# Kernel tuning notes

Hardware: AMD Instinct MI355X
Metric: run time of the kernel (lower is better)

## Reference

```python
import jax, jax.numpy as jnp
import numpy as np
import math

TOKEN_DIM = 1024
NUM_HEADS = 16
HEAD_DIM = TOKEN_DIM // NUM_HEADS
T, B, N = 32, 32, 64


def setup_inputs() -> dict:
    key = jax.random.key(0)
    ks = jax.random.split(key, 9)
    query_vec = jax.random.normal(ks[0], (T, B, TOKEN_DIM), dtype=jnp.float32)
    tokens = jax.random.normal(ks[1], (T, B, N, TOKEN_DIM), dtype=jnp.float32)
    gate_logits = jax.random.normal(ks[2], (T, B, N), dtype=jnp.float32)
    scale = 1.0 / math.sqrt(TOKEN_DIM)
    Wq = jax.random.normal(ks[3], (TOKEN_DIM, TOKEN_DIM), dtype=jnp.float32) * scale
    Wk = jax.random.normal(ks[4], (TOKEN_DIM, TOKEN_DIM), dtype=jnp.float32) * scale
    Wv = jax.random.normal(ks[5], (TOKEN_DIM, TOKEN_DIM), dtype=jnp.float32) * scale
    bq = jnp.zeros((TOKEN_DIM,), dtype=jnp.float32)
    bk = jnp.zeros((TOKEN_DIM,), dtype=jnp.float32)
    bv = jnp.zeros((TOKEN_DIM,), dtype=jnp.float32)
    return {"query_vec": query_vec, "tokens": tokens, "gate_logits": gate_logits,
            "Wq": Wq, "bq": bq, "Wk": Wk, "bk": bk, "Wv": Wv, "bv": bv}


def reference(query_vec, tokens, gate_logits, Wq, bq, Wk, bk, Wv, bv):
    # QKV projections
    q = query_vec @ Wq + bq                      # [T,B,D]
    k = tokens @ Wk + bk                         # [T,B,N,D]
    v = tokens @ Wv + bv                         # [T,B,N,D]
    q = q.reshape(T, B, NUM_HEADS, HEAD_DIM)
    k = k.reshape(T, B, N, NUM_HEADS, HEAD_DIM)
    v = v.reshape(T, B, N, NUM_HEADS, HEAD_DIM)
    logits = jnp.einsum('tbhd,tbnhd->tbhn', q, k) / math.sqrt(HEAD_DIM)
    logits = logits + gate_logits[:, :, None, :]
    attn = jax.nn.softmax(logits, axis=-1)       # [T,B,H,N]
    attended = jnp.einsum('tbhn,tbnhd->tbhd', attn, v)
    attended = attended.reshape(T, B, TOKEN_DIM)
    mean_attn = attn.mean(axis=2)                # [T,B,N]
    return (attended, mean_attn, logits)
```

## Files before the change

### kernel.cpp

```cpp
#include <hip/hip_runtime.h>
#include <hip/hip_bf16.h>
#include <hip/hip_cooperative_groups.h>

namespace cg = cooperative_groups;

typedef __attribute__((ext_vector_type(4))) float f32x4;
typedef __attribute__((ext_vector_type(8))) short bf16x8;
typedef unsigned int u32;
typedef unsigned short u16;

#define DEV static __device__ __forceinline__


DEV u16 f2bf(float x){
  union { float f; u32 u; } v; v.f = x;
  u32 r = v.u + 0x7FFFu + ((v.u >> 16) & 1u);
  return (u16)(r >> 16);
}
DEV float bf2f(u16 s){
  union { u32 u; float f; } v; v.u = ((u32)s) << 16;
  return v.f;
}

#define MFMA16(a,b,c) __builtin_amdgcn_mfma_f32_16x16x32_bf16((a),(b),(c),0,0,0)

DEV int tok_off(int n, int dbyte){ return n*2048 + (dbyte ^ ((n & 7) << 4)); }

#define MEGA_DYN_LDS 65536

__global__ __launch_bounds__(256, 2) void k_mega(
    const float* __restrict__ qv, const float* __restrict__ tokens,
    const float* __restrict__ gate,
    const float* __restrict__ Wq, const float* __restrict__ bq,
    const float* __restrict__ Wk, const float* __restrict__ bk,
    const float* __restrict__ Wv, const float* __restrict__ bv,
    u16* __restrict__ qvB, u16* __restrict__ WqT, u16* __restrict__ WkB,
    u16* __restrict__ WvT, float* __restrict__ qf, u16* __restrict__ qb,
    u16* __restrict__ U, u16* __restrict__ ctxb,
    float* __restrict__ out_att, float* __restrict__ out_mean,
    float* __restrict__ out_logits){
  extern __shared__ __align__(16) char smem[];
  __shared__ __align__(16) char sstat[10496];
  cg::grid_group grid = cg::this_grid();
  const int tid = threadIdx.x;
  const int bx  = blockIdx.x;
  const int l = tid & 63, w = tid >> 6, g = l >> 4, li = l & 15;

  {
    const f32x4* s4 = (const f32x4*)qv;
    uint2* d2 = (uint2*)qvB;
    int g0 = bx*256 + tid;
    #pragma unroll
    for (int i = 0; i < 2; ++i){
      int idx = g0 + i*131072;
      f32x4 v = s4[idx];
      uint2 pk;
      pk.x = (u32)f2bf(v.x) | ((u32)f2bf(v.y) << 16);
      pk.y = (u32)f2bf(v.z) | ((u32)f2bf(v.w) << 16);
      d2[idx] = pk;
    }
  }
  {
    u16 (*tile)[65] = (u16 (*)[65])sstat;
    for (int tl = bx; tl < 768; tl += 512){
      __syncthreads();
      const int which = tl >> 8, t8 = tl & 255;
      const float* src = which==0 ? Wq : (which==1 ? Wk : Wv);
      const int bi = (t8 >> 4) << 6, bj = (t8 & 15) << 6;
      #pragma unroll
      for (int k2 = 0; k2 < 16; ++k2){
        int e = tid + (k2 << 8); int r = e >> 6, c = e & 63;
        tile[r][c] = f2bf(src[(size_t)(bi + r)*1024 + bj + c]);
      }
      __syncthreads();
      if (which == 1){
        #pragma unroll
        for (int k2 = 0; k2 < 16; ++k2){
          int e = tid + (k2 << 8); int r = e >> 6, c = e & 63;
          WkB[(size_t)(bi + r)*1024 + bj + c] = tile[r][c];
        }
      } else {
        u16* dst = which==0 ? WqT : WvT;
        #pragma unroll
        for (int k2 = 0; k2 < 16; ++k2){
          int e = tid + (k2 << 8); int r = e >> 6, c = e & 63;
          dst[(size_t)(bj + r)*1024 + bi + c] = tile[c][r];
        }
      }
    }
  }
  __threadfence(); grid.sync(); __threadfence();

  {
    const int wm = w & 1, wn = w >> 1;
    const int m_base = (bx >> 5)*64 + wm*32;
    const int n_base = (bx & 31)*32 + wn*16;
    f32x4 acc[2]; acc[0] = (f32x4)0.0f; acc[1] = (f32x4)0.0f;
    #pragma unroll 4
    for (int kb = 0; kb < 32; ++kb){
      const int k0 = kb*32 + g*8;
      bf16x8 b = *(const bf16x8*)(WqT + (size_t)(n_base + li)*1024 + k0);
      #pragma unroll
      for (int rt = 0; rt < 2; ++rt){
        bf16x8 a = *(const bf16x8*)(qvB + (size_t)(m_base + rt*16 + li)*1024 + k0);
        acc[rt] = MFMA16(a, b, acc[rt]);
      }
    }
    #pragma unroll
    for (int rt = 0; rt < 2; ++rt)
      #pragma unroll
      for (int r = 0; r < 4; ++r){
        int m = m_base + rt*16 + g*4 + r;
        int n = n_base + li;
        float val = acc[rt][r] + bq[n];
        qf[(size_t)m*1024 + n] = val;
        qb[(size_t)m*1024 + n] = f2bf(val);
      }
  }
  __threadfence(); grid.sync(); __threadfence();

  {
    u16 (*stile)[64] = (u16 (*)[64])sstat;
    const int wm = w & 1, wn = w >> 1;
    for (int i = 0; i < 8; ++i){
      const int tl = bx*8 + i;
      const int tb0 = (tl >> 8)*64, d0 = ((tl >> 4) & 15)*64, h = tl & 15;
      f32x4 acc[2][2];
      #pragma unroll
      for (int a0=0;a0<2;++a0)
        #pragma unroll
        for (int b0=0;b0<2;++b0) acc[a0][b0] = (f32x4)0.0f;
      #pragma unroll
      for (int kb = 0; kb < 2; ++kb){
        const int k0 = h*64 + kb*32 + g*8;
        bf16x8 a[2], b[2];
        #pragma unroll
        for (int rt=0;rt<2;++rt)
          a[rt] = *(const bf16x8*)(qb + (size_t)(tb0 + wm*32 + rt*16 + li)*1024 + k0);
        #pragma unroll
        for (int ct=0;ct<2;++ct)
          b[ct] = *(const bf16x8*)(WkB + (size_t)(d0 + wn*32 + ct*16 + li)*1024 + k0);
        #pragma unroll
        for (int rt=0;rt<2;++rt)
          #pragma unroll
          for (int ct=0;ct<2;++ct)
            acc[rt][ct] = MFMA16(a[rt], b[ct], acc[rt][ct]);
      }
      __syncthreads();
      #pragma unroll
      for (int rt=0;rt<2;++rt)
        #pragma unroll
        for (int ct=0;ct<2;++ct)
          #pragma unroll
          for (int r=0;r<4;++r)
            stile[wm*32 + rt*16 + g*4 + r][wn*32 + ct*16 + li] = f2bf(acc[rt][ct][r]);
      __syncthreads();
      const int rr = tid >> 2, cg4 = tid & 3;
      f32x4* dst = (f32x4*)(U + ((size_t)(tb0 + rr)*16 + h)*1024 + d0 + cg4*16);
      const f32x4* s4 = (const f32x4*)(&stile[rr][cg4*16]);
      dst[0] = s4[0]; dst[1] = s4[1];
    }
  }
  __threadfence(); grid.sync(); __threadfence();

  {
    float* part_s   = (float*)(sstat);
    float* logits_s = (float*)(sstat + 4096);
    float* p_s      = (float*)(sstat + 8192);
    float* csum     = (float*)(sstat + 10240);
    float* r_s      = (float*)(sstat + 10304);
    float* mzs      = (float*)(sstat + 10368);
    const int nt = w & 1, kh = w >> 1;
    const int sh = tid >> 4, sj = tid & 15;

    __syncthreads();

    {
      const f32x4* src4 = (const f32x4*)(tokens + (size_t)bx*65536);
      f32x4 pstg[32];
      #pragma unroll
      for (int it = 0; it < 32; ++it) pstg[it] = src4[(size_t)it*256 + tid];
      #pragma unroll
      for (int it = 0; it < 32; ++it){
        f32x4 v = pstg[it];
        uint2 pk;
        pk.x = (u32)f2bf(v.x) | ((u32)f2bf(v.y) << 16);
        pk.y = (u32)f2bf(v.z) | ((u32)f2bf(v.w) << 16);
        *(uint2*)(smem + tok_off(it, tid*8)) = pk;
      }
    }

    float m_run = -1e30f, z_run = 0.0f;
    f32x4 cacc[4][4];

    for (int r = 0; r < 4; ++r){
      const int c = r & 1, n0 = c*32;
      const int tb = bx + (r >> 1)*512;

      if (c == 0){
        m_run = -1e30f; z_run = 0.0f;
        #pragma unroll
        for (int i=0;i<4;++i)
          #pragma unroll
          for (int j=0;j<4;++j) cacc[i][j] = (f32x4)0.0f;
        const float* qp = qf + (size_t)tb*1024 + sh*64 + sj*4;
        const float* bp = bk + sh*64 + sj*4;
        float part = qp[0]*bp[0] + qp[1]*bp[1] + qp[2]*bp[2] + qp[3]*bp[3];
        part += __shfl_xor(part, 1); part += __shfl_xor(part, 2);
        part += __shfl_xor(part, 4); part += __shfl_xor(part, 8);
        if (sj == 0) csum[sh] = part;
      }

      __syncthreads();

      {
        bf16x8 a[16];
        const bf16x8* Ub = (const bf16x8*)(U + (size_t)tb*16384);
        #pragma unroll
        for (int i = 0; i < 16; ++i)
          a[i] = Ub[li*128 + (kh*16 + i)*4 + g];
        f32x4 acc = (f32x4)0.0f;
        #pragma unroll
        for (int i = 0; i < 16; ++i){
          int kb = kh*16 + i;
          bf16x8 b = *(const bf16x8*)(smem + tok_off(nt*16 + li, (kb*32 + g*8)*2));
          acc = MFMA16(a[i], b, acc);
        }
        *(f32x4*)(part_s + (size_t)(w*64 + l)*4) = acc;
        __syncthreads();
        if (kh == 0){
          acc += *(const f32x4*)(part_s + (size_t)((w+2)*64 + l)*4);
          float gv = gate[(size_t)tb*64 + n0 + nt*16 + li];
          #pragma unroll
          for (int rg = 0; rg < 4; ++rg){
            int h = g*4 + rg;
            logits_s[h*64 + n0 + nt*16 + li] = (acc[rg] + csum[h])*0.125f + gv;
          }
        }
        __syncthreads();
      }

      f32x4 stg[32];
      const int rn = r + 1;
      if (rn < 4){
        const f32x4* srcn = (const f32x4*)(tokens + (size_t)(bx + (rn >> 1)*512)*65536);
        const int n0n = (rn & 1)*32;
        #pragma unroll
        for (int it = 0; it < 32; ++it)
          stg[it] = srcn[(size_t)(n0n + it)*256 + tid];
      }

      {
        float lv0 = logits_s[sh*64 + n0 + sj];
        float lv1 = logits_s[sh*64 + n0 + 16 + sj];
        out_logits[(size_t)tb*1024 + sh*64 + n0 + sj]      = lv0;
        out_logits[(size_t)tb*1024 + sh*64 + n0 + 16 + sj] = lv1;
        float cm = fmaxf(lv0, lv1);
        cm = fmaxf(cm, __shfl_xor(cm, 1)); cm = fmaxf(cm, __shfl_xor(cm, 2));
        cm = fmaxf(cm, __shfl_xor(cm, 4)); cm = fmaxf(cm, __shfl_xor(cm, 8));
        float m_new = fmaxf(m_run, cm);
        float rsc = __expf(m_run - m_new);
        float p0 = __expf(lv0 - m_new), p1 = __expf(lv1 - m_new);
        float zs = p0 + p1;
        zs += __shfl_xor(zs, 1); zs += __shfl_xor(zs, 2);
        zs += __shfl_xor(zs, 4); zs += __shfl_xor(zs, 8);
        z_run = z_run * rsc + zs;
        m_run = m_new;
        p_s[sj*16 + sh]        = p0;
        p_s[(sj + 16)*16 + sh] = p1;
        if (sj == 0){
          r_s[sh] = rsc;
          if (c == 1){ mzs[sh*2] = m_new; mzs[sh*2 + 1] = 1.0f / z_run; }
        }
      }
      __syncthreads();

      {
        float rr[4];
        #pragma unroll
        for (int hh = 0; hh < 4; ++hh) rr[hh] = r_s[w*4 + hh];
        #pragma unroll
        for (int dq = 0; dq < 4; ++dq)
          #pragma unroll
          for (int hh = 0; hh < 4; ++hh) cacc[dq][hh] *= rr[hh];
        for (int nl = 0; nl < 32; ++nl){
          f32x4 p = *(const f32x4*)(p_s + nl*16 + w*4);
          #pragma unroll
          for (int dq = 0; dq < 4; ++dq){
            uint2 t2 = *(const uint2*)(smem + tok_off(nl, (dq*256 + l*4)*2));
            float f0 = bf2f((u16)(t2.x & 0xFFFFu));
            float f1 = bf2f((u16)(t2.x >> 16));
            float f2 = bf2f((u16)(t2.y & 0xFFFFu));
            float f3 = bf2f((u16)(t2.y >> 16));
            #pragma unroll
            for (int hh = 0; hh < 4; ++hh){
              float av = p[hh];
              cacc[dq][hh].x += av*f0; cacc[dq][hh].y += av*f1;
              cacc[dq][hh].z += av*f2; cacc[dq][hh].w += av*f3;
            }
          }
        }
      }
      __syncthreads();

      if (rn < 4){
        #pragma unroll
        for (int it = 0; it < 32; ++it){
          f32x4 v = stg[it];
          uint2 pk;
          pk.x = (u32)f2bf(v.x) | ((u32)f2bf(v.y) << 16);
          pk.y = (u32)f2bf(v.z) | ((u32)f2bf(v.w) << 16);
          *(uint2*)(smem + tok_off(it, tid*8)) = pk;
        }
      }

      if (c == 1){
        if (tid < 64){
          float s = 0.0f;
          #pragma unroll
          for (int h = 0; h < 16; ++h)
            s += __expf(logits_s[h*64 + tid] - mzs[h*2]) * mzs[h*2 + 1];
          out_mean[(size_t)tb*64 + tid] = s * 0.0625f;
        }
        #pragma unroll
        for (int hh = 0; hh < 4; ++hh){
          const int h = w*4 + hh;
          const float zinv = mzs[h*2 + 1];
          #pragma unroll
          for (int dq = 0; dq < 4; ++dq){
            f32x4 v = cacc[dq][hh];
            uint2 pk;
            pk.x = (u32)f2bf(v.x * zinv) | ((u32)f2bf(v.y * zinv) << 16);
            pk.y = (u32)f2bf(v.z * zinv) | ((u32)f2bf(v.w * zinv) << 16);
            *(uint2*)(ctxb + ((size_t)tb*16 + h)*1024 + dq*256 + l*4) = pk;
          }
        }
      }
    }
  }
  __threadfence(); grid.sync(); __threadfence();

  {
    const int wm = w & 1, wn = w >> 1;
    const int m_base = (bx >> 4)*32, h = bx & 15;
    f32x4 acc[2]; acc[0] = (f32x4)0.0f; acc[1] = (f32x4)0.0f;
    #pragma unroll 4
    for (int kb = 0; kb < 32; ++kb){
      const int k0 = kb*32 + g*8;
      bf16x8 a = *(const bf16x8*)(ctxb + ((size_t)(m_base + wm*16 + li)*16 + h)*1024 + k0);
      #pragma unroll
      for (int ct = 0; ct < 2; ++ct){
        bf16x8 b = *(const bf16x8*)(WvT + (size_t)(h*64 + wn*32 + ct*16 + li)*1024 + k0);
        acc[ct] = MFMA16(a, b, acc[ct]);
      }
    }
    #pragma unroll
    for (int ct = 0; ct < 2; ++ct)
      #pragma unroll
      for (int r = 0; r < 4; ++r){
        int m = m_base + wm*16 + g*4 + r;
        int dout = h*64 + wn*32 + ct*16 + li;
        out_att[(size_t)m*1024 + dout] = acc[ct][r] + bv[dout];
      }
  }
}

__global__ __launch_bounds__(256) void k_convert(
    const float* __restrict__ Wq, const float* __restrict__ Wk, const float* __restrict__ Wv,
    u16* __restrict__ WqT, u16* __restrict__ WkB, u16* __restrict__ WvT){
  __shared__ u16 tile[64][65];
  const int which = blockIdx.y;
  const float* src = which==0 ? Wq : (which==1 ? Wk : Wv);
  const int bi = (blockIdx.x >> 4) << 6;
  const int bj = (blockIdx.x & 15) << 6;
  const int t  = threadIdx.x;
  #pragma unroll
  for (int k2 = 0; k2 < 16; ++k2){
    int e = t + (k2 << 8);
    int r = e >> 6, c = e & 63;
    tile[r][c] = f2bf(src[(size_t)(bi + r)*1024 + bj + c]);
  }
  __syncthreads();
  if (which == 1){
    #pragma unroll
    for (int k2 = 0; k2 < 16; ++k2){
      int e = t + (k2 << 8); int r = e >> 6, c = e & 63;
      WkB[(size_t)(bi + r)*1024 + bj + c] = tile[r][c];
    }
  } else {
    u16* dst = which==0 ? WqT : WvT;
    #pragma unroll
    for (int k2 = 0; k2 < 16; ++k2){
      int e = t + (k2 << 8); int r = e >> 6, c = e & 63;
      dst[(size_t)(bj + r)*1024 + bi + c] = tile[c][r];
    }
  }
}

__global__ __launch_bounds__(256) void k_qproj(
    const float* __restrict__ qv, const u16* __restrict__ WqT, const float* __restrict__ bq,
    float* __restrict__ qf, u16* __restrict__ qb){
  const int l = threadIdx.x & 63, w = threadIdx.x >> 6;
  const int wm = w & 1, wn = w >> 1;
  const int g = l >> 4, li = l & 15;
  const int m_base = blockIdx.x*64 + wm*32;
  const int n_base = blockIdx.y*64 + wn*32;
  f32x4 acc[2][2];
  #pragma unroll
  for (int i=0;i<2;++i)
    #pragma unroll
    for (int j=0;j<2;++j) acc[i][j] = (f32x4)0.0f;

  #pragma unroll 4
  for (int kb = 0; kb < 32; ++kb){
    const int k0 = kb*32 + g*8;
    bf16x8 a[2], b[2];
    #pragma unroll
    for (int rt = 0; rt < 2; ++rt){
      const float* p = qv + (size_t)(m_base + rt*16 + li)*1024 + k0;
      f32x4 lo = *(const f32x4*)p;
      f32x4 hi = *(const f32x4*)(p+4);
      union { u16 s[8]; bf16x8 v; } u;
      u.s[0]=f2bf(lo.x); u.s[1]=f2bf(lo.y); u.s[2]=f2bf(lo.z); u.s[3]=f2bf(lo.w);
      u.s[4]=f2bf(hi.x); u.s[5]=f2bf(hi.y); u.s[6]=f2bf(hi.z); u.s[7]=f2bf(hi.w);
      a[rt] = u.v;
    }
    #pragma unroll
    for (int ct = 0; ct < 2; ++ct)
      b[ct] = *(const bf16x8*)(WqT + (size_t)(n_base + ct*16 + li)*1024 + k0);
    #pragma unroll
    for (int rt = 0; rt < 2; ++rt)
      #pragma unroll
      for (int ct = 0; ct < 2; ++ct)
        acc[rt][ct] = MFMA16(a[rt], b[ct], acc[rt][ct]);
  }
  #pragma unroll
  for (int rt=0;rt<2;++rt)
    #pragma unroll
    for (int ct=0;ct<2;++ct)
      #pragma unroll
      for (int r=0;r<4;++r){
        int m = m_base + rt*16 + g*4 + r;
        int n = n_base + ct*16 + li;
        float val = acc[rt][ct][r] + bq[n];
        qf[(size_t)m*1024 + n] = val;
        qb[(size_t)m*1024 + n] = f2bf(val);
      }
}

__global__ __launch_bounds__(256) void k_umat(
    const u16* __restrict__ qb, const u16* __restrict__ WkB, u16* __restrict__ U){
  __shared__ __align__(16) u16 stile[64][64];
  const int l = threadIdx.x & 63, w = threadIdx.x >> 6;
  const int wm = w & 1, wn = w >> 1, g = l >> 4, li = l & 15;
  const int tb0 = blockIdx.x*64, d0 = blockIdx.y*64, h = blockIdx.z;
  f32x4 acc[2][2];
  #pragma unroll
  for (int i=0;i<2;++i)
    #pragma unroll
    for (int j=0;j<2;++j) acc[i][j] = (f32x4)0.0f;

  #pragma unroll
  for (int kb = 0; kb < 2; ++kb){
    const int k0 = h*64 + kb*32 + g*8;
    bf16x8 a[2], b[2];
    #pragma unroll
    for (int rt=0;rt<2;++rt)
      a[rt] = *(const bf16x8*)(qb + (size_t)(tb0 + wm*32 + rt*16 + li)*1024 + k0);
    #pragma unroll
    for (int ct=0;ct<2;++ct)
      b[ct] = *(const bf16x8*)(WkB + (size_t)(d0 + wn*32 + ct*16 + li)*1024 + k0);
    #pragma unroll
    for (int rt=0;rt<2;++rt)
      #pragma unroll
      for (int ct=0;ct<2;++ct)
        acc[rt][ct] = MFMA16(a[rt], b[ct], acc[rt][ct]);
  }
  #pragma unroll
  for (int rt=0;rt<2;++rt)
    #pragma unroll
    for (int ct=0;ct<2;++ct)
      #pragma unroll
      for (int r=0;r<4;++r)
        stile[wm*32 + rt*16 + g*4 + r][wn*32 + ct*16 + li] = f2bf(acc[rt][ct][r]);
  __syncthreads();
  const int r = threadIdx.x >> 2, cg4 = threadIdx.x & 3;
  f32x4* dst = (f32x4*)(U + ((size_t)(tb0 + r)*16 + h)*1024 + d0 + cg4*16);
  const f32x4* s4 = (const f32x4*)(&stile[r][cg4*16]);
  dst[0] = s4[0]; dst[1] = s4[1];
}

#define K3_LDS 76032
__global__ __launch_bounds__(256, 2) void k_attn(
    const float* __restrict__ tokens, const float* __restrict__ gate,
    const u16* __restrict__ U, const float* __restrict__ qf, const float* __restrict__ bk,
    float* __restrict__ out_logits, float* __restrict__ out_mean, u16* __restrict__ ctx){
  extern __shared__ __align__(16) char smem[];
  float* part_s   = (float*)(smem + 65536);
  float* logits_s = (float*)(smem + 69632);
  float* p_s      = (float*)(smem + 73728);
  float* csum     = (float*)(smem + 75776);
  float* r_s      = (float*)(smem + 75840);
  float* mzs      = (float*)(smem + 75904);
  const int tb = blockIdx.x;
  const int tid = threadIdx.x;
  const int l = tid & 63, w = tid >> 6, g = l >> 4, li = l & 15;
  const int nt = w & 1, kh = w >> 1;
  const int sh = tid >> 4, sj = tid & 15;

  bf16x8 a[16];
  const bf16x8* Ub = (const bf16x8*)(U + (size_t)tb*16384);
  #pragma unroll
  for (int i = 0; i < 16; ++i)
    a[i] = Ub[li*128 + (kh*16 + i)*4 + g];

  {
    const float* qp = qf + (size_t)tb*1024 + sh*64 + sj*4;
    const float* bp = bk + sh*64 + sj*4;
    float part = qp[0]*bp[0] + qp[1]*bp[1] + qp[2]*bp[2] + qp[3]*bp[3];
    part += __shfl_xor(part, 1); part += __shfl_xor(part, 2);
    part += __shfl_xor(part, 4); part += __shfl_xor(part, 8);
    if (sj == 0) csum[sh] = part;
  }

  float m_run = -1e30f, z_run = 0.0f;
  f32x4 cacc[4][4];
  #pragma unroll
  for (int i=0;i<4;++i)
    #pragma unroll
    for (int j=0;j<4;++j) cacc[i][j] = (f32x4)0.0f;

  const f32x4* src4 = (const f32x4*)(tokens + (size_t)tb*65536);

  for (int c = 0; c < 2; ++c){
    const int n0 = c*32;
    __syncthreads();
    #pragma unroll 8
    for (int it = 0; it < 32; ++it){
      f32x4 v = src4[(size_t)(n0 + it)*256 + tid];
      uint2 pk;
      pk.x = (u32)f2bf(v.x) | ((u32)f2bf(v.y) << 16);
      pk.y = (u32)f2bf(v.z) | ((u32)f2bf(v.w) << 16);
      *(uint2*)(smem + tok_off(it, tid*8)) = pk;
    }
    __syncthreads();
    {
      f32x4 acc = (f32x4)0.0f;
      #pragma unroll
      for (int i = 0; i < 16; ++i){
        int kb = kh*16 + i;
        bf16x8 b = *(const bf16x8*)(smem + tok_off(nt*16 + li, (kb*32 + g*8)*2));
        acc = MFMA16(a[i], b, acc);
      }
      *(f32x4*)(part_s + (size_t)(w*64 + l)*4) = acc;
      __syncthreads();
      if (kh == 0){
        acc += *(const f32x4*)(part_s + (size_t)((w+2)*64 + l)*4);
        float gv = gate[(size_t)tb*64 + n0 + nt*16 + li];
        #pragma unroll
        for (int r = 0; r < 4; ++r){
          int h = g*4 + r;
          logits_s[h*64 + n0 + nt*16 + li] = (acc[r] + csum[h])*0.125f + gv;
        }
      }
      __syncthreads();
    }
    {
      float lv0 = logits_s[sh*64 + n0 + sj];
      float lv1 = logits_s[sh*64 + n0 + 16 + sj];
      out_logits[(size_t)tb*1024 + sh*64 + n0 + sj]      = lv0;
      out_logits[(size_t)tb*1024 + sh*64 + n0 + 16 + sj] = lv1;
      float cm = fmaxf(lv0, lv1);
      cm = fmaxf(cm, __shfl_xor(cm, 1)); cm = fmaxf(cm, __shfl_xor(cm, 2));
      cm = fmaxf(cm, __shfl_xor(cm, 4)); cm = fmaxf(cm, __shfl_xor(cm, 8));
      float m_new = fmaxf(m_run, cm);
      float rsc = __expf(m_run - m_new);
      float p0 = __expf(lv0 - m_new), p1 = __expf(lv1 - m_new);
      float zs = p0 + p1;
      zs += __shfl_xor(zs, 1); zs += __shfl_xor(zs, 2);
      zs += __shfl_xor(zs, 4); zs += __shfl_xor(zs, 8);
      z_run = z_run * rsc + zs;
      m_run = m_new;
      p_s[sj*16 + sh]        = p0;
      p_s[(sj + 16)*16 + sh] = p1;
      if (sj == 0){
        r_s[sh] = rsc;
        if (c == 1){ mzs[sh*2] = m_new; mzs[sh*2 + 1] = 1.0f / z_run; }
      }
    }
    __syncthreads();
    {
      float rr[4];
      #pragma unroll
      for (int hh = 0; hh < 4; ++hh) rr[hh] = r_s[w*4 + hh];
      #pragma unroll
      for (int dq = 0; dq < 4; ++dq)
        #pragma unroll
        for (int hh = 0; hh < 4; ++hh) cacc[dq][hh] *= rr[hh];
      for (int nl = 0; nl < 32; ++nl){
        f32x4 p = *(const f32x4*)(p_s + nl*16 + w*4);
        #pragma unroll
        for (int dq = 0; dq < 4; ++dq){
          uint2 t2 = *(const uint2*)(smem + tok_off(nl, (dq*256 + l*4)*2));
          float f0 = bf2f((u16)(t2.x & 0xFFFFu));
          float f1 = bf2f((u16)(t2.x >> 16));
          float f2 = bf2f((u16)(t2.y & 0xFFFFu));
          float f3 = bf2f((u16)(t2.y >> 16));
          #pragma unroll
          for (int hh = 0; hh < 4; ++hh){
            float av = p[hh];
            cacc[dq][hh].x += av*f0; cacc[dq][hh].y += av*f1;
            cacc[dq][hh].z += av*f2; cacc[dq][hh].w += av*f3;
          }
        }
      }
    }
  }

  if (tid < 64){
    float s = 0.0f;
    #pragma unroll
    for (int h = 0; h < 16; ++h)
      s += __expf(logits_s[h*64 + tid] - mzs[h*2]) * mzs[h*2 + 1];
    out_mean[(size_t)tb*64 + tid] = s * 0.0625f;
  }

  #pragma unroll
  for (int hh = 0; hh < 4; ++hh){
    const int h = w*4 + hh;
    const float zinv = mzs[h*2 + 1];
    #pragma unroll
    for (int dq = 0; dq < 4; ++dq){
      f32x4 v = cacc[dq][hh];
      uint2 pk;
      pk.x = (u32)f2bf(v.x * zinv) | ((u32)f2bf(v.y * zinv) << 16);
      pk.y = (u32)f2bf(v.z * zinv) | ((u32)f2bf(v.w * zinv) << 16);
      *(uint2*)(ctx + ((size_t)tb*16 + h)*1024 + dq*256 + l*4) = pk;
    }
  }
}

__global__ __launch_bounds__(256) void k_attended(
    const u16* __restrict__ ctx, const u16* __restrict__ WvT, const float* __restrict__ bv,
    float* __restrict__ out_att){
  const int l = threadIdx.x & 63, w = threadIdx.x >> 6;
  const int wm = w & 1, wn = w >> 1, g = l >> 4, li = l & 15;
  const int tb0 = blockIdx.x*64, h = blockIdx.y;
  f32x4 acc[2][2];
  #pragma unroll
  for (int i=0;i<2;++i)
    #pragma unroll
    for (int j=0;j<2;++j) acc[i][j] = (f32x4)0.0f;

  #pragma unroll 4
  for (int kb = 0; kb < 32; ++kb){
    const int k0 = kb*32 + g*8;
    bf16x8 a[2], b[2];
    #pragma unroll
    for (int rt=0;rt<2;++rt)
      a[rt] = *(const bf16x8*)(ctx + ((size_t)(tb0 + wm*32 + rt*16 + li)*16 + h)*1024 + k0);
    #pragma unroll
    for (int ct=0;ct<2;++ct)
      b[ct] = *(const bf16x8*)(WvT + (size_t)(h*64 + wn*32 + ct*16 + li)*1024 + k0);
    #pragma unroll
    for (int rt=0;rt<2;++rt)
      #pragma unroll
      for (int ct=0;ct<2;++ct)
        acc[rt][ct] = MFMA16(a[rt], b[ct], acc[rt][ct]);
  }
  #pragma unroll
  for (int rt=0;rt<2;++rt)
    #pragma unroll
    for (int ct=0;ct<2;++ct)
      #pragma unroll
      for (int r=0;r<4;++r){
        int m = tb0 + wm*32 + rt*16 + g*4 + r;
        int dout = h*64 + wn*32 + ct*16 + li;
        out_att[(size_t)m*1024 + dout] = acc[rt][ct][r] + bv[dout];
      }
}

extern "C" void kernel_launch(void* const* d_in, const int* in_sizes, int n_in,
                              void* d_out, int out_size, void* d_ws, size_t ws_size,
                              hipStream_t stream){
  const float* qv     = (const float*)d_in[0];
  const float* tokens = (const float*)d_in[1];
  const float* gate   = (const float*)d_in[2];
  const float* Wq     = (const float*)d_in[3];
  const float* bq     = (const float*)d_in[4];
  const float* Wk     = (const float*)d_in[5];
  const float* bk     = (const float*)d_in[6];
  const float* Wv     = (const float*)d_in[7];
  const float* bv     = (const float*)d_in[8];

  char* ws = (char*)d_ws;
  u16*   qvB = (u16*)(ws);
  u16*   WqT = (u16*)(ws + (2u<<20));
  u16*   WkB = (u16*)(ws + (4u<<20));
  u16*   WvT = (u16*)(ws + (6u<<20));
  float* qf  = (float*)(ws + (8u<<20));
  u16*   qb  = (u16*)(ws + (12u<<20));
  u16*   U   = (u16*)(ws + (14u<<20));
  u16*   ctxb= (u16*)(ws + (46u<<20));

  float* out_att    = (float*)d_out;
  float* out_mean   = out_att + 1048576;
  float* out_logits = out_att + 1114112;

  int dev = 0; (void)hipGetDevice(&dev);
  int coop = 0; (void)hipDeviceGetAttribute(&coop, hipDeviceAttributeCooperativeLaunch, dev);
  int ncu = 0;  (void)hipDeviceGetAttribute(&ncu, hipDeviceAttributeMultiprocessorCount, dev);
  int perCU = 0;
  hipError_t oe = hipOccupancyMaxActiveBlocksPerMultiprocessor(
                      &perCU, (const void*)k_mega, 256, (size_t)MEGA_DYN_LDS);
  bool use_coop = (coop != 0) && (oe == hipSuccess) && ((long)perCU * (long)ncu >= 512);

  if (use_coop){
    void* args[] = { (void*)&qv, (void*)&tokens, (void*)&gate,
                     (void*)&Wq, (void*)&bq, (void*)&Wk, (void*)&bk,
                     (void*)&Wv, (void*)&bv,
                     (void*)&qvB, (void*)&WqT, (void*)&WkB, (void*)&WvT,
                     (void*)&qf, (void*)&qb, (void*)&U, (void*)&ctxb,
                     (void*)&out_att, (void*)&out_mean, (void*)&out_logits };
    hipError_t le = hipLaunchCooperativeKernel((const void*)k_mega, dim3(512), dim3(256),
                                               args, MEGA_DYN_LDS, stream);
    if (le == hipSuccess) return;
    use_coop = false;
  }

  (void)hipFuncSetAttribute((const void*)k_attn,
                            hipFuncAttributeMaxDynamicSharedMemorySize, K3_LDS);
  k_convert <<<dim3(256, 3),    256, 0,      stream>>>(Wq, Wk, Wv, WqT, WkB, WvT);
  k_qproj   <<<dim3(16, 16),    256, 0,      stream>>>(qv, WqT, bq, qf, qb);
  k_umat    <<<dim3(16, 16, 16),256, 0,      stream>>>(qb, WkB, U);
  k_attn    <<<dim3(1024),      256, K3_LDS, stream>>>(tokens, gate, U, qf, bk,
                                                       out_logits, out_mean, ctxb);
  k_attended<<<dim3(16, 16),    256, 0,      stream>>>(ctxb, WvT, bv, out_att);
}
```

Baseline: 174.8 us.

## Double-buffer token tiles in 16-row chunks and hoist U fragment loads

The attention phase now processes each token row block in four 16-token chunks instead of two 32-token chunks. Tiles are double-buffered in shared memory, so one __syncthreads per iteration goes away and the next chunk's global load is issued at the top of the loop, pinned there with sched barriers. The logits MFMA is split across all four waves along K, and each wave's U fragments load once per row block instead of once per chunk. This cuts staging registers and adds prefetch overlap, at the cost of twice as many loop iterations and barriers per token.

```diff
diff --git a/kernel.cpp b/kernel.cpp
--- a/kernel.cpp
+++ b/kernel.cpp
@@ -170,18 +170,17 @@
     float* csum     = (float*)(sstat + 10240);
     float* r_s      = (float*)(sstat + 10304);
     float* mzs      = (float*)(sstat + 10368);
-    const int nt = w & 1, kh = w >> 1;
     const int sh = tid >> 4, sj = tid & 15;
 
     __syncthreads();
 
     {
       const f32x4* src4 = (const f32x4*)(tokens + (size_t)bx*65536);
-      f32x4 pstg[32];
-      #pragma unroll
-      for (int it = 0; it < 32; ++it) pstg[it] = src4[(size_t)it*256 + tid];
-      #pragma unroll
-      for (int it = 0; it < 32; ++it){
+      f32x4 pstg[16];
+      #pragma unroll
+      for (int it = 0; it < 16; ++it) pstg[it] = src4[(size_t)it*256 + tid];
+      #pragma unroll
+      for (int it = 0; it < 16; ++it){
         f32x4 v = pstg[it];
         uint2 pk;
         pk.x = (u32)f2bf(v.x) | ((u32)f2bf(v.y) << 16);
@@ -192,10 +191,24 @@
 
     float m_run = -1e30f, z_run = 0.0f;
     f32x4 cacc[4][4];
-
-    for (int r = 0; r < 4; ++r){
-      const int c = r & 1, n0 = c*32;
-      const int tb = bx + (r >> 1)*512;
+    bf16x8 a[8];
+
+    for (int r = 0; r < 8; ++r){
+      const int c = r & 3, n0 = c*16;
+      const int tb = bx + (r >> 2)*512;
+      char* bufc = smem + (size_t)(r & 1)*32768;
+
+      f32x4 stg[16];
+      const int rn = r + 1;
+      if (rn < 8){
+        const f32x4* srcn = (const f32x4*)(tokens
+            + (size_t)(bx + (rn >> 2)*512)*65536 + (size_t)((rn & 3)*16)*1024);
+        #pragma unroll
+        for (int it = 0; it < 16; ++it)
+          stg[it] = srcn[(size_t)it*256 + tid];
+        __builtin_amdgcn_sched_barrier(0);
+      }
+      __builtin_amdgcn_sched_barrier(0);
 
       if (c == 0){
         m_run = -1e30f; z_run = 0.0f;
@@ -203,6 +216,10 @@
         for (int i=0;i<4;++i)
           #pragma unroll
           for (int j=0;j<4;++j) cacc[i][j] = (f32x4)0.0f;
+        const bf16x8* Ub = (const bf16x8*)(U + (size_t)tb*16384);
+        #pragma unroll
+        for (int i = 0; i < 8; ++i)
+          a[i] = Ub[li*128 + (w*8 + i)*4 + g];
         const float* qp = qf + (size_t)tb*1024 + sh*64 + sj*4;
         const float* bp = bk + sh*64 + sj*4;
         float part = qp[0]*bp[0] + qp[1]*bp[1] + qp[2]*bp[2] + qp[3]*bp[3];
@@ -214,80 +231,63 @@
       __syncthreads();
 
       {
-        bf16x8 a[16];
-        const bf16x8* Ub = (const bf16x8*)(U + (size_t)tb*16384);
-        #pragma unroll
-        for (int i = 0; i < 16; ++i)
-          a[i] = Ub[li*128 + (kh*16 + i)*4 + g];
         f32x4 acc = (f32x4)0.0f;
         #pragma unroll
-        for (int i = 0; i < 16; ++i){
-          int kb = kh*16 + i;
-          bf16x8 b = *(const bf16x8*)(smem + tok_off(nt*16 + li, (kb*32 + g*8)*2));
+        for (int i = 0; i < 8; ++i){
+          bf16x8 b = *(const bf16x8*)(bufc + tok_off(li, ((w*8 + i)*32 + g*8)*2));
           acc = MFMA16(a[i], b, acc);
         }
         *(f32x4*)(part_s + (size_t)(w*64 + l)*4) = acc;
         __syncthreads();
-        if (kh == 0){
-          acc += *(const f32x4*)(part_s + (size_t)((w+2)*64 + l)*4);
-          float gv = gate[(size_t)tb*64 + n0 + nt*16 + li];
+        if (w == 0){
+          acc += *(const f32x4*)(part_s + (size_t)(64  + l)*4);
+          acc += *(const f32x4*)(part_s + (size_t)(128 + l)*4);
+          acc += *(const f32x4*)(part_s + (size_t)(192 + l)*4);
+          float gv = gate[(size_t)tb*64 + n0 + li];
           #pragma unroll
           for (int rg = 0; rg < 4; ++rg){
             int h = g*4 + rg;
-            logits_s[h*64 + n0 + nt*16 + li] = (acc[rg] + csum[h])*0.125f + gv;
+            logits_s[h*64 + n0 + li] = (acc[rg] + csum[h])*0.125f + gv;
           }
         }
         __syncthreads();
       }
 
-      f32x4 stg[32];
-      const int rn = r + 1;
-      if (rn < 4){
-        const f32x4* srcn = (const f32x4*)(tokens + (size_t)(bx + (rn >> 1)*512)*65536);
-        const int n0n = (rn & 1)*32;
-        #pragma unroll
-        for (int it = 0; it < 32; ++it)
-          stg[it] = srcn[(size_t)(n0n + it)*256 + tid];
-      }
-
       {
-        float lv0 = logits_s[sh*64 + n0 + sj];
-        float lv1 = logits_s[sh*64 + n0 + 16 + sj];
-        out_logits[(size_t)tb*1024 + sh*64 + n0 + sj]      = lv0;
-        out_logits[(size_t)tb*1024 + sh*64 + n0 + 16 + sj] = lv1;
-        float cm = fmaxf(lv0, lv1);
+        float lv = logits_s[sh*64 + n0 + sj];
+        out_logits[(size_t)tb*1024 + sh*64 + n0 + sj] = lv;
+        float cm = lv;
         cm = fmaxf(cm, __shfl_xor(cm, 1)); cm = fmaxf(cm, __shfl_xor(cm, 2));
         cm = fmaxf(cm, __shfl_xor(cm, 4)); cm = fmaxf(cm, __shfl_xor(cm, 8));
         float m_new = fmaxf(m_run, cm);
         float rsc = __expf(m_run - m_new);
-        float p0 = __expf(lv0 - m_new), p1 = __expf(lv1 - m_new);
-        float zs = p0 + p1;
+        float p0 = __expf(lv - m_new);
+        float zs = p0;
         zs += __shfl_xor(zs, 1); zs += __shfl_xor(zs, 2);
         zs += __shfl_xor(zs, 4); zs += __shfl_xor(zs, 8);
         z_run = z_run * rsc + zs;
         m_run = m_new;
-        p_s[sj*16 + sh]        = p0;
-        p_s[(sj + 16)*16 + sh] = p1;
+        p_s[sj*16 + sh] = p0;
         if (sj == 0){
           r_s[sh] = rsc;
-          if (c == 1){ mzs[sh*2] = m_new; mzs[sh*2 + 1] = 1.0f / z_run; }
+          if (c == 3){ mzs[sh*2] = m_new; mzs[sh*2 + 1] = 1.0f / z_run; }
         }
       }
       __syncthreads();
 
       {
-        float rr[4];
-        #pragma unroll
-        for (int hh = 0; hh < 4; ++hh) rr[hh] = r_s[w*4 + hh];
+        float rr4[4];
+        #pragma unroll
+        for (int hh = 0; hh < 4; ++hh) rr4[hh] = r_s[w*4 + hh];
         #pragma unroll
         for (int dq = 0; dq < 4; ++dq)
           #pragma unroll
-          for (int hh = 0; hh < 4; ++hh) cacc[dq][hh] *= rr[hh];
-        for (int nl = 0; nl < 32; ++nl){
+          for (int hh = 0; hh < 4; ++hh) cacc[dq][hh] *= rr4[hh];
+        for (int nl = 0; nl < 16; ++nl){
           f32x4 p = *(const f32x4*)(p_s + nl*16 + w*4);
           #pragma unroll
           for (int dq = 0; dq < 4; ++dq){
-            uint2 t2 = *(const uint2*)(smem + tok_off(nl, (dq*256 + l*4)*2));
+            uint2 t2 = *(const uint2*)(bufc + tok_off(nl, (dq*256 + l*4)*2));
             float f0 = bf2f((u16)(t2.x & 0xFFFFu));
             float f1 = bf2f((u16)(t2.x >> 16));
             float f2 = bf2f((u16)(t2.y & 0xFFFFu));
@@ -301,20 +301,20 @@
           }
         }
       }
-      __syncthreads();
-
-      if (rn < 4){
-        #pragma unroll
-        for (int it = 0; it < 32; ++it){
+
+      if (rn < 8){
+        char* bufn = smem + (size_t)(rn & 1)*32768;
+        #pragma unroll
+        for (int it = 0; it < 16; ++it){
           f32x4 v = stg[it];
           uint2 pk;
           pk.x = (u32)f2bf(v.x) | ((u32)f2bf(v.y) << 16);
           pk.y = (u32)f2bf(v.z) | ((u32)f2bf(v.w) << 16);
-          *(uint2*)(smem + tok_off(it, tid*8)) = pk;
-        }
-      }
-
-      if (c == 1){
+          *(uint2*)(bufn + tok_off(it, tid*8)) = pk;
+        }
+      }
+
+      if (c == 3){
         if (tid < 64){
           float s = 0.0f;
           #pragma unroll
```

New measurement: 177.4 us. No clear change (+1.5%).
